# Kernel optimization log

Measured on AMD Instinct MI355X. Metric: run time of the kernel, lower is better.

## Reference

```python
import jax, jax.numpy as jnp
import numpy as np

N_E = 8192
E_DIM = 255  # spatial dim; full Lorentz dim = E_DIM + 1
BETA = 0.25
EPS = 1e-7


def _rand_lorentz(key, n, d):
    """Sample n points on the Lorentz manifold (curvature c=1), radii in [1,6]."""
    k1, k2 = jax.random.split(key)
    radii = jax.random.uniform(k1, (n, 1)) * 5.0 + 1.0
    t = jnp.cosh(radii)  # time component, >= cosh(1)
    dirs = jax.random.normal(k2, (n, d))
    dirs = dirs / jnp.linalg.norm(dirs, axis=-1, keepdims=True)
    s = dirs * jnp.sqrt(jnp.maximum(t ** 2 - 1.0, 1e-7))
    return jnp.concatenate([t, s], axis=-1)


def setup_inputs() -> dict:
    key = jax.random.key(0)
    k_u, k_cb = jax.random.split(key)
    B, H, W = 8, 32, 32
    u = _rand_lorentz(k_u, B * H * W, E_DIM).reshape(B, H, W, E_DIM + 1)
    codebook = _rand_lorentz(k_cb, N_E, E_DIM)
    return {"u_hyp": u, "codebook": codebook}


def reference(u_hyp, codebook):
    shape = u_hyp.shape
    d_full = E_DIM + 1
    u = u_hyp.reshape(-1, d_full)          # [N, D]
    n = u.shape[0]
    # Minkowski metric signs: (-, +, +, ..., +)
    signs = jnp.concatenate([-jnp.ones((1,), u.dtype), jnp.ones((E_DIM,), u.dtype)])

    # Lorentzian inner products with all codes: <u, c>_L = -u0*c0 + u_s . c_s
    K = (u * signs) @ codebook.T           # [N, n_e]
    dist = jnp.arccosh(jnp.maximum(-K, 1.0 + EPS))  # hyperbolic distance (c=1)
    idx = jnp.argmin(dist, axis=-1)        # [N]
    x_q = codebook[idx]                    # [N, D] gather

    def pdist(a, b):  # elementwise Lorentzian distance
        inner = jnp.sum(a * b * signs, axis=-1)
        return jnp.arccosh(jnp.maximum(-inner, 1.0 + EPS))

    sg = jax.lax.stop_gradient
    codebook_loss = pdist(sg(u), x_q).mean()
    commitment_loss = pdist(u, sg(x_q)).mean()
    loss = codebook_loss + BETA * commitment_loss

    # straight-through estimator
    z_q = (u + sg(x_q - u)).reshape(shape)

    counts = jnp.zeros((N_E,), u.dtype).at[idx].add(1.0)
    e_mean = counts / n
    entropy = -jnp.sum(e_mean * jnp.log(e_mean + 1e-10))
    perplexity = jnp.exp(entropy)
    diversity_loss = entropy
    return loss, z_q, perplexity, diversity_loss, e_mean
```

## Files before the change

kernel.cpp:

```cpp
#include <hip/hip_runtime.h>
#include <hip/hip_bf16.h>
#include <stdint.h>

#define N_PTS   8192
#define D       256
#define N_E     8192
#define BETA    0.25f
#define EPS_1   1.0000001f

typedef unsigned long long u64;
typedef __attribute__((ext_vector_type(8))) short bf16x8;
typedef __attribute__((ext_vector_type(8))) short short8;
typedef __attribute__((ext_vector_type(4))) float f32x4;

#define WS_KEYS   0
#define WS_COUNTS (N_PTS * 8)
#define WS_LOSS   (WS_COUNTS + N_E * 4)
#define WS_AHI    (1 << 20)
#define WS_ALO    (WS_AHI + N_PTS * D * 2)
#define WS_BHI    (WS_ALO + N_PTS * D * 2)
#define WS_BLO    (WS_BHI + N_E * D * 2)

__device__ __forceinline__ short f2bf(float x) {
    __hip_bfloat16 h = __float2bfloat16(x);
    return *reinterpret_cast<short*>(&h);
}
__device__ __forceinline__ float bf2f(short s) {
    __hip_bfloat16 h = *reinterpret_cast<__hip_bfloat16*>(&s);
    return __bfloat162float(h);
}

#define GLOAD16(gp, lp) __builtin_amdgcn_global_load_lds(                      \
    (const __attribute__((address_space(1))) void*)(gp),                       \
    (__attribute__((address_space(3))) void*)(lp), 16, 0, 0)

#define DPP_MIN(x, ctrl)                                                       \
    x = fminf(x, __int_as_float(__builtin_amdgcn_update_dpp(                   \
            __float_as_int(x), __float_as_int(x), (ctrl), 0xF, 0xF, true)))

__global__ __launch_bounds__(256) void k_prep(
    const float* __restrict__ u, const float* __restrict__ cb,
    short* __restrict__ Ahi, short* __restrict__ Alo,
    short* __restrict__ Bhi, short* __restrict__ Blo,
    u64* __restrict__ keys, float* __restrict__ counts,
    double* __restrict__ loss_sum)
{
    const int tid = blockIdx.x * 256 + threadIdx.x;
    if (tid < N_E)   counts[tid] = 0.f;
    if (tid < N_PTS) keys[tid] = ~0ULL;
    if (tid == 0)    *loss_sum = 0.0;

    const int blk = tid >> 6;
    const int l   = tid & 63;
    const int s   = blk >> 3, c = blk & 7;
    const int p   = s * 16 + (l & 15);
    const int k   = c * 32 + (l >> 4) * 8;
    const size_t gin  = (size_t)p * D + k;
    const size_t gout = (size_t)tid * 8;

    float v[8];
    short8 h8, l8;

    *(float4*)&v[0] = *(const float4*)&u[gin];
    *(float4*)&v[4] = *(const float4*)&u[gin + 4];
    if (k == 0) v[0] = -v[0];
    #pragma unroll
    for (int j = 0; j < 8; ++j) {
        h8[j] = f2bf(v[j]);
        l8[j] = f2bf(v[j] - bf2f(h8[j]));
    }
    *(short8*)&Ahi[gout] = h8;
    *(short8*)&Alo[gout] = l8;

    *(float4*)&v[0] = *(const float4*)&cb[gin];
    *(float4*)&v[4] = *(const float4*)&cb[gin + 4];
    #pragma unroll
    for (int j = 0; j < 8; ++j) {
        h8[j] = f2bf(v[j]);
        l8[j] = f2bf(v[j] - bf2f(h8[j]));
    }
    *(short8*)&Bhi[gout] = h8;
    *(short8*)&Blo[gout] = l8;
}

#define BMM 128
#define BNN 128
#define NKS (D / 32)

__global__ __launch_bounds__(256, 4) void k_argmin_mfma(
    const short* __restrict__ Ahi, const short* __restrict__ Alo,
    const short* __restrict__ Bhi, const short* __restrict__ Blo,
    u64* __restrict__ keys)
{
    __shared__ short sm[4][8 * 512];

    const int t   = threadIdx.x;
    const int w   = t >> 6;
    const int l   = t & 63;
    const int rb  = blockIdx.x >> 6;
    const int cbk = blockIdx.x & 63;
    const int r0  = rb * BMM, c0 = cbk * BNN;
    const int wr  = w >> 1, wc = w & 1;

    const short* gsrc = (w == 0) ? Ahi : (w == 1) ? Alo : (w == 2) ? Bhi : Blo;
    short* ldst = sm[w];
    const int s0 = ((w < 2) ? rb : cbk) * 8;

    f32x4 acc[4][4];
    #pragma unroll
    for (int i = 0; i < 4; ++i)
        #pragma unroll
        for (int j = 0; j < 4; ++j) acc[i][j] = (f32x4){0.f, 0.f, 0.f, 0.f};

    for (int kk = 0; kk < NKS; ++kk) {
        __syncthreads();
        #pragma unroll
        for (int i = 0; i < 8; ++i)
            GLOAD16(gsrc + (size_t)((s0 + i) * 8 + kk) * 512 + l * 8,
                    ldst + i * 512);
        __syncthreads();

        bf16x8 ah[4], al[4], bh[4], bl[4];
        #pragma unroll
        for (int f = 0; f < 4; ++f) {
            ah[f] = *(const bf16x8*)&sm[0][(wr * 4 + f) * 512 + l * 8];
            al[f] = *(const bf16x8*)&sm[1][(wr * 4 + f) * 512 + l * 8];
            bh[f] = *(const bf16x8*)&sm[2][(wc * 4 + f) * 512 + l * 8];
            bl[f] = *(const bf16x8*)&sm[3][(wc * 4 + f) * 512 + l * 8];
        }
        #pragma unroll
        for (int mf = 0; mf < 4; ++mf)
            #pragma unroll
            for (int nf = 0; nf < 4; ++nf) {
                acc[mf][nf] = __builtin_amdgcn_mfma_f32_16x16x32_bf16(
                    ah[mf], bh[nf], acc[mf][nf], 0, 0, 0);
                acc[mf][nf] = __builtin_amdgcn_mfma_f32_16x16x32_bf16(
                    ah[mf], bl[nf], acc[mf][nf], 0, 0, 0);
                acc[mf][nf] = __builtin_amdgcn_mfma_f32_16x16x32_bf16(
                    al[mf], bh[nf], acc[mf][nf], 0, 0, 0);
            }
    }

    const int g  = l >> 4;
    const int cc = l & 15;
    #pragma unroll
    for (int mf = 0; mf < 4; ++mf) {
        #pragma unroll
        for (int r = 0; r < 4; ++r) {
            float mm = fmaxf(-acc[mf][0][r], EPS_1);
            unsigned code = (unsigned)(c0 + wc * 64 + cc);
            #pragma unroll
            for (int nf = 1; nf < 4; ++nf) {
                float mv = fmaxf(-acc[mf][nf][r], EPS_1);
                if (mv < mm) { mm = mv; code = (unsigned)(c0 + wc * 64 + nf * 16 + cc); }
            }
            float mv = mm;
            DPP_MIN(mv, 0xB1);
            DPP_MIN(mv, 0x4E);
            DPP_MIN(mv, 0x141);
            DPP_MIN(mv, 0x140);
            if (mm == mv) {
                const int row = r0 + wr * 64 + mf * 16 + g * 4 + r;
                u64 key = ((u64)__float_as_uint(mm) << 32) | code;
                atomicMin(&keys[row], key);
            }
        }
    }
}

__global__ __launch_bounds__(256) void k_gather(
    const float* __restrict__ u, const float* __restrict__ cb,
    const u64* __restrict__ keys, float* __restrict__ out,
    float* __restrict__ counts, double* __restrict__ loss_sum)
{
    __shared__ float sred[4];
    const int t    = threadIdx.x;
    const int w    = t >> 6;
    const int row  = blockIdx.x * 4 + w;
    const int lane = t & 63;
    const u64 key  = keys[row];
    const int idx  = (int)(unsigned)(key & 0xffffffffULL);

    float* zq = out + 1;
    float4 uv = *(const float4*)&u[(size_t)row * D + lane * 4];
    float4 cv = *(const float4*)&cb[(size_t)idx * D + lane * 4];
    if (lane == 0) uv.x = -uv.x;
    float partial = uv.x * cv.x + uv.y * cv.y + uv.z * cv.z + uv.w * cv.w;
    *(float4*)&zq[(size_t)row * D + lane * 4] = cv;

    #pragma unroll
    for (int s = 32; s >= 1; s >>= 1)
        partial += __shfl_xor(partial, s);

    if (lane == 0) {
        float m = fmaxf(-partial, EPS_1);
        sred[w] = acoshf(m);
        atomicAdd(&counts[idx], 1.f);
    }
    __syncthreads();
    if (t == 0)
        atomicAdd(loss_sum, (double)(sred[0] + sred[1] + sred[2] + sred[3]));
}

__global__ __launch_bounds__(256) void k_final(
    const float* __restrict__ counts, const double* __restrict__ loss_sum,
    float* __restrict__ out)
{
    __shared__ float red[256];
    const int t = threadIdx.x;
    const int OFF_P = 1 + N_PTS * D;
    float ent = 0.f;
    for (int i = t; i < N_E; i += 256) {
        float e = counts[i] * (1.0f / N_PTS);
        out[OFF_P + 2 + i] = e;
        ent -= e * logf(e + 1e-10f);
    }
    red[t] = ent;
    __syncthreads();
    for (int s = 128; s > 0; s >>= 1) {
        if (t < s) red[t] += red[t + s];
        __syncthreads();
    }
    if (t == 0) {
        float entropy = red[0];
        out[0]         = (1.0f + BETA) * (float)(*loss_sum / (double)N_PTS);
        out[OFF_P]     = expf(entropy);
        out[OFF_P + 1] = entropy;
    }
}

extern "C" void kernel_launch(void* const* d_in, const int* in_sizes, int n_in,
                              void* d_out, int out_size, void* d_ws, size_t ws_size,
                              hipStream_t stream)
{
    const float* u  = (const float*)d_in[0];
    const float* cb = (const float*)d_in[1];
    float* out = (float*)d_out;
    char* ws = (char*)d_ws;

    u64*    keys     = (u64*)(ws + WS_KEYS);
    float*  counts   = (float*)(ws + WS_COUNTS);
    double* loss_sum = (double*)(ws + WS_LOSS);
    short*  Ahi = (short*)(ws + WS_AHI);
    short*  Alo = (short*)(ws + WS_ALO);
    short*  Bhi = (short*)(ws + WS_BHI);
    short*  Blo = (short*)(ws + WS_BLO);

    k_prep<<<N_PTS * D / 8 / 256, 256, 0, stream>>>(u, cb, Ahi, Alo, Bhi, Blo,
                                                    keys, counts, loss_sum);
    k_argmin_mfma<<<(N_PTS / BMM) * (N_E / BNN), 256, 0, stream>>>(
        Ahi, Alo, Bhi, Blo, keys);
    k_gather<<<N_PTS / 4, 256, 0, stream>>>(u, cb, keys, out, counts, loss_sum);
    k_final<<<1, 256, 0, stream>>>(counts, loss_sum, out);
}
```

Baseline: 151.1 us.

## Fuse gather and final reduction into argmin kernel via last-block counters

Removes the separate gather and final kernels. The last block to finish each row-block gathers codebook rows, computes the distance losses and counts for its 128 rows, and the last row-block to finish computes entropy and the scalar outputs. This saves two kernel launches and their dependency gaps, and lets the gather tail overlap with remaining GEMM blocks. The cost is atomic counters, threadfences, and serialized tail work inside a few blocks.

```diff
diff --git a/kernel.cpp b/kernel.cpp
--- a/kernel.cpp
+++ b/kernel.cpp
@@ -13,13 +13,15 @@
 typedef __attribute__((ext_vector_type(8))) short short8;
 typedef __attribute__((ext_vector_type(4))) float f32x4;
 
-#define WS_KEYS   0
-#define WS_COUNTS (N_PTS * 8)
-#define WS_LOSS   (WS_COUNTS + N_E * 4)
-#define WS_AHI    (1 << 20)
-#define WS_ALO    (WS_AHI + N_PTS * D * 2)
-#define WS_BHI    (WS_ALO + N_PTS * D * 2)
-#define WS_BLO    (WS_BHI + N_E * D * 2)
+#define WS_KEYS    0
+#define WS_COUNTS  (N_PTS * 8)
+#define WS_LOSS    (WS_COUNTS + N_E * 4)
+#define WS_RB_DONE (WS_LOSS + 16)
+#define WS_GDONE   (WS_RB_DONE + 64 * 4)
+#define WS_AHI     (1 << 20)
+#define WS_ALO     (WS_AHI + N_PTS * D * 2)
+#define WS_BHI     (WS_ALO + N_PTS * D * 2)
+#define WS_BLO     (WS_BHI + N_E * D * 2)
 
 __device__ __forceinline__ short f2bf(float x) {
     __hip_bfloat16 h = __float2bfloat16(x);
@@ -43,12 +45,15 @@
     short* __restrict__ Ahi, short* __restrict__ Alo,
     short* __restrict__ Bhi, short* __restrict__ Blo,
     u64* __restrict__ keys, float* __restrict__ counts,
-    double* __restrict__ loss_sum)
+    double* __restrict__ loss_sum, unsigned* __restrict__ rb_done,
+    unsigned* __restrict__ gdone)
 {
     const int tid = blockIdx.x * 256 + threadIdx.x;
     if (tid < N_E)   counts[tid] = 0.f;
     if (tid < N_PTS) keys[tid] = ~0ULL;
     if (tid == 0)    *loss_sum = 0.0;
+    if (tid < 64)    rb_done[tid] = 0u;
+    if (tid == 64)   *gdone = 0u;
 
     const int blk = tid >> 6;
     const int l   = tid & 63;
@@ -90,9 +95,14 @@
 __global__ __launch_bounds__(256, 4) void k_argmin_mfma(
     const short* __restrict__ Ahi, const short* __restrict__ Alo,
     const short* __restrict__ Bhi, const short* __restrict__ Blo,
-    u64* __restrict__ keys)
+    u64* __restrict__ keys,
+    const float* __restrict__ u, const float* __restrict__ cb,
+    float* __restrict__ out, float* __restrict__ counts,
+    double* __restrict__ loss_sum, unsigned* __restrict__ rb_done,
+    unsigned* __restrict__ gdone)
 {
     __shared__ short sm[4][8 * 512];
+    __shared__ int   sflag;
 
     const int t   = threadIdx.x;
     const int w   = t >> 6;
@@ -166,52 +176,57 @@
             }
         }
     }
-}
-
-__global__ __launch_bounds__(256) void k_gather(
-    const float* __restrict__ u, const float* __restrict__ cb,
-    const u64* __restrict__ keys, float* __restrict__ out,
-    float* __restrict__ counts, double* __restrict__ loss_sum)
-{
-    __shared__ float sred[4];
-    const int t    = threadIdx.x;
-    const int w    = t >> 6;
-    const int row  = blockIdx.x * 4 + w;
-    const int lane = t & 63;
-    const u64 key  = keys[row];
-    const int idx  = (int)(unsigned)(key & 0xffffffffULL);
+
+    __syncthreads();
+    if (t == 0) {
+        __threadfence();
+        sflag = (atomicAdd(&rb_done[rb], 1u) == 63u);
+    }
+    __syncthreads();
+    if (!sflag) return;
+    __threadfence();
+
+    u64* smk = (u64*)&sm[0][0];
+    if (t < BMM)
+        smk[t] = atomicMin(&keys[r0 + t], ~0ULL);
+    __syncthreads();
 
     float* zq = out + 1;
-    float4 uv = *(const float4*)&u[(size_t)row * D + lane * 4];
-    float4 cv = *(const float4*)&cb[(size_t)idx * D + lane * 4];
-    if (lane == 0) uv.x = -uv.x;
-    float partial = uv.x * cv.x + uv.y * cv.y + uv.z * cv.z + uv.w * cv.w;
-    *(float4*)&zq[(size_t)row * D + lane * 4] = cv;
-
-    #pragma unroll
-    for (int s = 32; s >= 1; s >>= 1)
-        partial += __shfl_xor(partial, s);
-
-    if (lane == 0) {
-        float m = fmaxf(-partial, EPS_1);
-        sred[w] = acoshf(m);
-        atomicAdd(&counts[idx], 1.f);
-    }
-    __syncthreads();
-    if (t == 0)
-        atomicAdd(loss_sum, (double)(sred[0] + sred[1] + sred[2] + sred[3]));
-}
-
-__global__ __launch_bounds__(256) void k_final(
-    const float* __restrict__ counts, const double* __restrict__ loss_sum,
-    float* __restrict__ out)
-{
-    __shared__ float red[256];
-    const int t = threadIdx.x;
+    float fsum = 0.f;
+    for (int rr = 0; rr < 32; ++rr) {
+        const int lrow = w * 32 + rr;
+        const int row  = r0 + lrow;
+        const int idx  = (int)(unsigned)(smk[lrow] & 0xffffffffULL);
+        float4 uv = *(const float4*)&u[(size_t)row * D + l * 4];
+        float4 cv = *(const float4*)&cb[(size_t)idx * D + l * 4];
+        if (l == 0) uv.x = -uv.x;
+        float partial = uv.x * cv.x + uv.y * cv.y + uv.z * cv.z + uv.w * cv.w;
+        *(float4*)&zq[(size_t)row * D + l * 4] = cv;
+        #pragma unroll
+        for (int s = 32; s >= 1; s >>= 1)
+            partial += __shfl_xor(partial, s);
+        if (l == 0) {
+            fsum += acoshf(fmaxf(-partial, EPS_1));
+            atomicAdd(&counts[idx], 1.f);
+        }
+    }
+    if (l == 0) atomicAdd(loss_sum, (double)fsum);
+
+    __syncthreads();
+    if (t == 0) {
+        __threadfence();
+        sflag = (atomicAdd(gdone, 1u) == 63u);
+    }
+    __syncthreads();
+    if (!sflag) return;
+    __threadfence();
+
+    float* red = (float*)&sm[1][0];
     const int OFF_P = 1 + N_PTS * D;
     float ent = 0.f;
     for (int i = t; i < N_E; i += 256) {
-        float e = counts[i] * (1.0f / N_PTS);
+        float cv_ = atomicAdd(&counts[i], 0.f);
+        float e = cv_ * (1.0f / N_PTS);
         out[OFF_P + 2 + i] = e;
         ent -= e * logf(e + 1e-10f);
     }
@@ -223,7 +238,8 @@
     }
     if (t == 0) {
         float entropy = red[0];
-        out[0]         = (1.0f + BETA) * (float)(*loss_sum / (double)N_PTS);
+        double ls = atomicAdd(loss_sum, 0.0);
+        out[0]         = (1.0f + BETA) * (float)(ls / (double)N_PTS);
         out[OFF_P]     = expf(entropy);
         out[OFF_P + 1] = entropy;
     }
@@ -238,18 +254,18 @@
     float* out = (float*)d_out;
     char* ws = (char*)d_ws;
 
-    u64*    keys     = (u64*)(ws + WS_KEYS);
-    float*  counts   = (float*)(ws + WS_COUNTS);
-    double* loss_sum = (double*)(ws + WS_LOSS);
-    short*  Ahi = (short*)(ws + WS_AHI);
-    short*  Alo = (short*)(ws + WS_ALO);
-    short*  Bhi = (short*)(ws + WS_BHI);
-    short*  Blo = (short*)(ws + WS_BLO);
-
-    k_prep<<<N_PTS * D / 8 / 256, 256, 0, stream>>>(u, cb, Ahi, Alo, Bhi, Blo,
-                                                    keys, counts, loss_sum);
+    u64*      keys     = (u64*)(ws + WS_KEYS);
+    float*    counts   = (float*)(ws + WS_COUNTS);
+    double*   loss_sum = (double*)(ws + WS_LOSS);
+    unsigned* rb_done  = (unsigned*)(ws + WS_RB_DONE);
+    unsigned* gdone    = (unsigned*)(ws + WS_GDONE);
+    short*    Ahi = (short*)(ws + WS_AHI);
+    short*    Alo = (short*)(ws + WS_ALO);
+    short*    Bhi = (short*)(ws + WS_BHI);
+    short*    Blo = (short*)(ws + WS_BLO);
+
+    k_prep<<<N_PTS * D / 8 / 256, 256, 0, stream>>>(
+        u, cb, Ahi, Alo, Bhi, Blo, keys, counts, loss_sum, rb_done, gdone);
     k_argmin_mfma<<<(N_PTS / BMM) * (N_E / BNN), 256, 0, stream>>>(
-        Ahi, Alo, Bhi, Blo, keys);
-    k_gather<<<N_PTS / 4, 256, 0, stream>>>(u, cb, keys, out, counts, loss_sum);
-    k_final<<<1, 256, 0, stream>>>(counts, loss_sum, out);
-}
+        Ahi, Alo, Bhi, Blo, keys, u, cb, out, counts, loss_sum, rb_done, gdone);
+}
```

After: 377.3 us. +149.7%, slower.
